# Performance work log

Measured on AMD Instinct MI355X. Metric: run time of the kernel, lower is better.

## Reference

```python
import jax, jax.numpy as jnp
import numpy as np

VOCAB, POS_V, NER_V, DEPREL_V = 50000, 50, 10, 40
EMB, POS_D, NER_D, MEM = 300, 30, 30, 200
NUM_LAYERS = 2


def setup_inputs() -> dict:
    key = jax.random.key(0)
    ks = jax.random.split(key, 12)
    B, L = 32, 100
    adj = jax.random.randint(ks[0], (B, L, L), 0, DEPREL_V)
    words = jax.random.randint(ks[1], (B, L), 0, VOCAB)
    pos = jax.random.randint(ks[2], (B, L), 0, POS_V)
    ner = jax.random.randint(ks[3], (B, L), 0, NER_V)
    s = 0.02
    emb = jax.random.normal(ks[4], (VOCAB, EMB), jnp.float32) * s
    pos_emb = jax.random.normal(ks[5], (POS_V, POS_D), jnp.float32) * s
    ner_emb = jax.random.normal(ks[6], (NER_V, NER_D), jnp.float32) * s
    deprel_emb = jax.random.normal(ks[7], (DEPREL_V, MEM), jnp.float32) * s
    deprel_emb = deprel_emb.at[0].set(0.0)  # padding_idx=0
    in_dim = EMB + POS_D + NER_D
    Wp = jax.random.normal(ks[8], (MEM, in_dim), jnp.float32) * s
    bp = jnp.zeros((MEM,), jnp.float32)
    W0 = jax.random.normal(ks[9], (MEM, MEM), jnp.float32) * s
    b0 = jnp.zeros((MEM,), jnp.float32)
    W1 = jax.random.normal(ks[10], (MEM, MEM), jnp.float32) * s
    b1 = jnp.zeros((MEM,), jnp.float32)
    return {"adj": adj, "words": words, "pos": pos, "ner": ner,
            "emb": emb, "pos_emb": pos_emb, "ner_emb": ner_emb,
            "deprel_emb": deprel_emb, "Wp": Wp, "bp": bp,
            "W0": W0, "b0": b0, "W1": W1, "b1": b1}


def reference(adj, words, pos, ner, emb, pos_emb, ner_emb, deprel_emb,
              Wp, bp, W0, b0, W1, b1):
    # embedding lookups + concat  -> [B, L, in_dim]
    embs = jnp.concatenate([emb[words], pos_emb[pos], ner_emb[ner]], axis=-1)
    # preprocessor linear (diagonal_deprel branch)  -> [B, L, D]
    x = embs @ Wp.T + bp
    # per-edge relation embedding gather  -> [B, L, L, D]
    deprel_adj = deprel_emb[adj]
    adj_m = (adj != 0).astype(jnp.float32)            # [B, L, L]
    denom = adj_m.sum(2)[..., None] + 1.0             # [B, L, 1]
    mask = ((adj_m.sum(2) + adj_m.sum(1)) == 0)[..., None]  # [B, L, 1]
    for W, b in ((W0, b0), (W1, b1)):
        # diagonal deprel aggregation: (deprel_adj * x[:,None]) summed over neighbors
        Ax = jnp.einsum('blmd,bmd->bld', deprel_adj, x)
        AxW = (Ax @ W.T + b) + (x @ W.T + b)
        x = jax.nn.relu(AxW / denom)
    return x, mask
```

## Files before the change

### kernel.cpp

```cpp
#include <hip/hip_runtime.h>
#include <hip/hip_bf16.h>

#define BB 32
#define LL 100
#define DD 200
#define KIN 360
#define NP (BB*LL)
#define RNUM 40
#define LT 13
#define NT 8

__device__ __forceinline__ void fma4(float4& a, const float4& w, float s) {
    a.x = fmaf(w.x, s, a.x);
    a.y = fmaf(w.y, s, a.y);
    a.z = fmaf(w.z, s, a.z);
    a.w = fmaf(w.w, s, a.w);
}
__device__ __forceinline__ unsigned bf16rn(float f) {
    unsigned u = __float_as_uint(f);
    return (u + 0x7fffu + ((u >> 16) & 1u)) >> 16;
}
__device__ __forceinline__ unsigned pk2(float a, float b) {
    return bf16rn(a) | (bf16rn(b) << 16);
}
__device__ __forceinline__ float lo16(unsigned u) { return __uint_as_float(u << 16); }
__device__ __forceinline__ float hi16(unsigned u) { return __uint_as_float(u & 0xffff0000u); }

__global__ __launch_bounds__(256) void prep_transpose_kernel(
        const int* __restrict__ adj,
        const float* __restrict__ Wp, const float* __restrict__ W0, const float* __restrict__ W1,
        float* __restrict__ WpT, float* __restrict__ W0T, float* __restrict__ W1T,
        float* __restrict__ invd, float* __restrict__ mask_out) {
    int bid = blockIdx.x, tid = threadIdx.x;
    if (bid < 25) {
        int t = bid * 256 + tid;
        int half = t & 1;
        int pl = t >> 1;
        int b = pl / LL, l = pl % LL;
        const int4* row = (const int4*)(adj + (size_t)pl * LL);
        int q0 = half ? 13 : 0, q1 = half ? 25 : 13;
        int rc = 0;
        for (int i = q0; i < q1; ++i) {
            int4 a = row[i];
            rc += (a.x != 0) + (a.y != 0) + (a.z != 0) + (a.w != 0);
        }
        const int* base = adj + (size_t)b * LL * LL + l;
        int cc = 0;
        for (int m = half * 50; m < half * 50 + 50; ++m) cc += (base[(size_t)m * LL] != 0);
        rc += __shfl_xor(rc, 1);
        cc += __shfl_xor(cc, 1);
        if (!half) {
            invd[pl] = 1.0f / (float)(rc + 1);
            mask_out[pl] = (rc + cc == 0) ? 1.0f : 0.0f;
        }
    } else {
        int i = (bid - 25) * 256 + tid;
        if (i < 18000) {
            int k = i / 50, o = (i % 50) * 4;
            float4 v;
            v.x = Wp[(size_t)(o + 0) * KIN + k];
            v.y = Wp[(size_t)(o + 1) * KIN + k];
            v.z = Wp[(size_t)(o + 2) * KIN + k];
            v.w = Wp[(size_t)(o + 3) * KIN + k];
            ((float4*)WpT)[i] = v;
        } else if (i < 28000) {
            int q = i - 18000;
            int k = q / 50, o = (q % 50) * 4;
            float4 v;
            v.x = W0[(size_t)(o + 0) * DD + k];
            v.y = W0[(size_t)(o + 1) * DD + k];
            v.z = W0[(size_t)(o + 2) * DD + k];
            v.w = W0[(size_t)(o + 3) * DD + k];
            ((float4*)W0T)[q] = v;
        } else if (i < 38000) {
            int q = i - 28000;
            int k = q / 50, o = (q % 50) * 4;
            float4 v;
            v.x = W1[(size_t)(o + 0) * DD + k];
            v.y = W1[(size_t)(o + 1) * DD + k];
            v.z = W1[(size_t)(o + 2) * DD + k];
            v.w = W1[(size_t)(o + 3) * DD + k];
            ((float4*)W1T)[q] = v;
        }
    }
}

__global__ __launch_bounds__(256) void embed_gemv_kernel(
        const int* __restrict__ words, const int* __restrict__ pos, const int* __restrict__ ner,
        const float* __restrict__ emb, const float* __restrict__ pose, const float* __restrict__ nere,
        const float* __restrict__ wpt, const float* __restrict__ bp,
        float* __restrict__ xA) {
    __shared__ float es[8 * KIN];
    __shared__ float4 red[4 * 8 * 50];
    int tid = threadIdx.x;
    int pbase = blockIdx.x * 8;

    float2* es2 = (float2*)es;
    for (int idx = tid; idx < 8 * 180; idx += 256) {
        int p = idx / 180, j2 = idx % 180;
        int gp = pbase + p;
        float2 v;
        if (j2 < 150)      v = ((const float2*)emb)[(size_t)words[gp] * 150 + j2];
        else if (j2 < 165) v = ((const float2*)pose)[pos[gp] * 15 + (j2 - 150)];
        else               v = ((const float2*)nere)[ner[gp] * 15 + (j2 - 165)];
        es2[idx] = v;
    }
    __syncthreads();

    int lane = tid & 63, w = tid >> 6;
    bool act = lane < 50;
    int oq = act ? lane : 49;
    int kq0 = w * 24;
    int npair = (w < 3) ? 12 : 9;
    int kqlast = kq0 + 2 * npair - 1;
    const float4* wt4 = (const float4*)wpt;
    const float4* es4 = (const float4*)es;

    float4 a[8];
    #pragma unroll
    for (int p = 0; p < 8; ++p) a[p] = make_float4(0.f, 0.f, 0.f, 0.f);

    float4 wc[8], wn[8];
    #pragma unroll
    for (int q = 0; q < 2; ++q)
        #pragma unroll
        for (int j = 0; j < 4; ++j)
            wc[q * 4 + j] = wt4[(size_t)(4 * (kq0 + q) + j) * 50 + oq];

    for (int pr = 0; pr < npair; ++pr) {
        int nb = kq0 + 2 * pr + 2;
        int nbA = nb <= kqlast ? nb : kq0;
        int nbB = nb + 1 <= kqlast ? nb + 1 : kq0;
        #pragma unroll
        for (int j = 0; j < 4; ++j) wn[j]     = wt4[(size_t)(4 * nbA + j) * 50 + oq];
        #pragma unroll
        for (int j = 0; j < 4; ++j) wn[4 + j] = wt4[(size_t)(4 * nbB + j) * 50 + oq];
        #pragma unroll
        for (int q = 0; q < 2; ++q) {
            int kq = kq0 + 2 * pr + q;
            #pragma unroll
            for (int p = 0; p < 8; ++p) {
                float4 s = es4[p * 90 + kq];
                fma4(a[p], wc[q * 4 + 0], s.x); fma4(a[p], wc[q * 4 + 1], s.y);
                fma4(a[p], wc[q * 4 + 2], s.z); fma4(a[p], wc[q * 4 + 3], s.w);
            }
        }
        #pragma unroll
        for (int j = 0; j < 8; ++j) wc[j] = wn[j];
    }

    if (act) {
        #pragma unroll
        for (int p = 0; p < 8; ++p) red[w * 400 + p * 50 + oq] = a[p];
    }
    __syncthreads();
    for (int t = tid; t < 400; t += 256) {
        int oq2 = t % 50;
        float4 v0 = red[t], v1 = red[400 + t], v2 = red[800 + t], v3 = red[1200 + t];
        float4 bb = ((const float4*)bp)[oq2];
        float4 v;
        v.x = v0.x + v1.x + v2.x + v3.x + bb.x;
        v.y = v0.y + v1.y + v2.y + v3.y + bb.y;
        v.z = v0.z + v1.z + v2.z + v3.z + bb.z;
        v.w = v0.w + v1.w + v2.w + v3.w + bb.w;
        ((float4*)xA)[(size_t)(pbase + t / 50) * 50 + oq2] = v;
    }
}

__global__ __launch_bounds__(512) void layer_kernel(
        const float* __restrict__ x, const int* __restrict__ adj,
        const float* __restrict__ deprel, const float* __restrict__ wt,
        const float* __restrict__ bias, const float* __restrict__ invd,
        float* __restrict__ out) {
    __shared__ uint2 deps_b[RNUM * 50];
    __shared__ unsigned adjp[LT * 25];
    __shared__ float4 Sh[2 * 650];
    __shared__ float4 Sfin[650];
    int b = blockIdx.y, tile = blockIdx.x;
    int l0 = tile * LT;
    int lcnt = min(LT, LL - l0);
    int tid = threadIdx.x;
    const float4* x4 = (const float4*)x;

    for (int i = tid; i < RNUM * 50; i += 512) {
        float4 v = ((const float4*)deprel)[i];
        deps_b[i] = make_uint2(pk2(v.x, v.y), pk2(v.z, v.w));
    }
    for (int i = tid; i < lcnt * 25; i += 512) {
        int li = i / 25, mg = i % 25;
        int4 a = ((const int4*)(adj + (size_t)(b * LL + l0 + li) * LL))[mg];
        adjp[i] = (unsigned)a.x | ((unsigned)a.y << 8) | ((unsigned)a.z << 16) | ((unsigned)a.w << 24);
    }
    __syncthreads();

    int lane = tid & 63, w = tid >> 6;
    int lg = w & 3, mh = w >> 2;
    bool act = lane < 50;
    int dq = lane;

    float4 acc[4];
    #pragma unroll
    for (int i = 0; i < 4; ++i) acc[i] = make_float4(0.f, 0.f, 0.f, 0.f);
    if (act) {
        int mg0 = mh ? 13 : 0, mg1 = mh ? 25 : 13;
        float4 xc[4], xn[4];
        #pragma unroll
        for (int mm = 0; mm < 4; ++mm)
            xc[mm] = x4[(size_t)(b * LL + 4 * mg0 + mm) * 50 + dq];
        for (int mg = mg0; mg < mg1; ++mg) {
            int mgn = (mg + 1 < mg1) ? mg + 1 : mg;
            #pragma unroll
            for (int mm = 0; mm < 4; ++mm)
                xn[mm] = x4[(size_t)(b * LL + 4 * mgn + mm) * 50 + dq];
            unsigned ap[4];
            #pragma unroll
            for (int i = 0; i < 4; ++i) {
                int li = lg + 4 * i;
                ap[i] = (li < lcnt) ? adjp[li * 25 + mg] : 0u;
            }
            #pragma unroll
            for (int mm = 0; mm < 4; ++mm) {
                #pragma unroll
                for (int i = 0; i < 4; ++i) {
                    unsigned r = (ap[i] >> (8 * mm)) & 0xffu;
                    uint2 dv = deps_b[r * 50 + dq];
                    acc[i].x = fmaf(lo16(dv.x), xc[mm].x, acc[i].x);
                    acc[i].y = fmaf(hi16(dv.x), xc[mm].y, acc[i].y);
                    acc[i].z = fmaf(lo16(dv.y), xc[mm].z, acc[i].z);
                    acc[i].w = fmaf(hi16(dv.y), xc[mm].w, acc[i].w);
                }
            }
            #pragma unroll
            for (int mm = 0; mm < 4; ++mm) xc[mm] = xn[mm];
        }
        #pragma unroll
        for (int i = 0; i < 4; ++i) {
            int li = lg + 4 * i;
            if (li < lcnt) Sh[mh * 650 + li * 50 + dq] = acc[i];
        }
    }
    __syncthreads();

    for (int t2 = tid; t2 < 650; t2 += 512) {
        int li = t2 / 50;
        if (li < lcnt) {
            float4 s0 = Sh[t2], s1 = Sh[650 + t2];
            float4 xr = x4[(size_t)(b * LL + l0 + li) * 50 + (t2 % 50)];
            float4 s;
            s.x = s0.x + s1.x + xr.x; s.y = s0.y + s1.y + xr.y;
            s.z = s0.z + s1.z + xr.z; s.w = s0.w + s1.w + xr.w;
            Sfin[t2] = s;
        }
    }
    __syncthreads();

    const float4* wt4 = (const float4*)wt;
    int oq = act ? lane : 49;
    int kq0 = mh * 25;
    float4 ba[4];
    #pragma unroll
    for (int i = 0; i < 4; ++i) ba[i] = make_float4(0.f, 0.f, 0.f, 0.f);

    float4 wc[8], wn[8];
    #pragma unroll
    for (int q = 0; q < 2; ++q)
        #pragma unroll
        for (int j = 0; j < 4; ++j)
            wc[q * 4 + j] = wt4[(size_t)(4 * (kq0 + q) + j) * 50 + oq];

    int lic[4];
    #pragma unroll
    for (int i = 0; i < 4; ++i) {
        int li = lg + 4 * i;
        lic[i] = li < lcnt ? li : lcnt - 1;
    }

    for (int pr = 0; pr < 12; ++pr) {
        int nb = kq0 + 2 * pr + 2;
        int nbB = (nb + 1 <= kq0 + 24) ? nb + 1 : kq0;
        #pragma unroll
        for (int j = 0; j < 4; ++j) wn[j]     = wt4[(size_t)(4 * nb + j) * 50 + oq];
        #pragma unroll
        for (int j = 0; j < 4; ++j) wn[4 + j] = wt4[(size_t)(4 * nbB + j) * 50 + oq];
        #pragma unroll
        for (int q = 0; q < 2; ++q) {
            int kq = kq0 + 2 * pr + q;
            #pragma unroll
            for (int i = 0; i < 4; ++i) {
                float4 s = Sfin[lic[i] * 50 + kq];
                fma4(ba[i], wc[q * 4 + 0], s.x); fma4(ba[i], wc[q * 4 + 1], s.y);
                fma4(ba[i], wc[q * 4 + 2], s.z); fma4(ba[i], wc[q * 4 + 3], s.w);
            }
        }
        #pragma unroll
        for (int j = 0; j < 8; ++j) wc[j] = wn[j];
    }
    {
        int kq = kq0 + 24;
        #pragma unroll
        for (int i = 0; i < 4; ++i) {
            float4 s = Sfin[lic[i] * 50 + kq];
            fma4(ba[i], wc[0], s.x); fma4(ba[i], wc[1], s.y);
            fma4(ba[i], wc[2], s.z); fma4(ba[i], wc[3], s.w);
        }
    }

    if (act) {
        #pragma unroll
        for (int i = 0; i < 4; ++i) {
            int li = lg + 4 * i;
            if (li < lcnt) Sh[mh * 650 + li * 50 + oq] = ba[i];
        }
    }
    __syncthreads();

    for (int t2 = tid; t2 < 650; t2 += 512) {
        int li = t2 / 50, oq2 = t2 % 50;
        if (li < lcnt) {
            float4 v0 = Sh[t2], v1 = Sh[650 + t2];
            float4 bb = ((const float4*)bias)[oq2];
            int p = b * LL + l0 + li;
            float sc = invd[p];
            float4 v;
            v.x = fmaxf((v0.x + v1.x + 2.f * bb.x) * sc, 0.f);
            v.y = fmaxf((v0.y + v1.y + 2.f * bb.y) * sc, 0.f);
            v.z = fmaxf((v0.z + v1.z + 2.f * bb.z) * sc, 0.f);
            v.w = fmaxf((v0.w + v1.w + 2.f * bb.w) * sc, 0.f);
            ((float4*)out)[(size_t)p * 50 + oq2] = v;
        }
    }
}

extern "C" void kernel_launch(void* const* d_in, const int* in_sizes, int n_in,
                              void* d_out, int out_size, void* d_ws, size_t ws_size,
                              hipStream_t stream) {
    const int*   adj   = (const int*)d_in[0];
    const int*   words = (const int*)d_in[1];
    const int*   pos   = (const int*)d_in[2];
    const int*   ner   = (const int*)d_in[3];
    const float* emb   = (const float*)d_in[4];
    const float* pose  = (const float*)d_in[5];
    const float* nere  = (const float*)d_in[6];
    const float* dep   = (const float*)d_in[7];
    const float* Wp    = (const float*)d_in[8];
    const float* bp    = (const float*)d_in[9];
    const float* W0    = (const float*)d_in[10];
    const float* b0    = (const float*)d_in[11];
    const float* W1    = (const float*)d_in[12];
    const float* b1    = (const float*)d_in[13];
    float* out = (float*)d_out;
    float* ws  = (float*)d_ws;

    float* xA   = ws;
    float* xB   = ws + 640000;
    float* WpT  = ws + 1280000;
    float* W0T  = ws + 1352000;
    float* W1T  = ws + 1392000;
    float* invd = ws + 1432000;

    prep_transpose_kernel<<<25 + 149, 256, 0, stream>>>(adj, Wp, W0, W1, WpT, W0T, W1T,
                                                        invd, out + (size_t)NP * DD);
    embed_gemv_kernel<<<NP / 8, 256, 0, stream>>>(words, pos, ner, emb, pose, nere,
                                                  WpT, bp, xA);
    layer_kernel<<<dim3(NT, BB), 512, 0, stream>>>(xA, adj, dep, W0T, b0, invd, xB);
    layer_kernel<<<dim3(NT, BB), 512, 0, stream>>>(xB, adj, dep, W1T, b1, invd, out);
}
```

Measured before the change: 74.09 us.

## Double block sizes and split reductions across more wavefronts in embed and layer kernels

Embed GEMV blocks grow from 256 to 512 threads, splitting the K dimension over 8 wavefronts instead of 4, with an 8-way shared-memory reduction. Layer blocks grow from 512 to 1024 threads, splitting the neighbor aggregation and the weight GEMV over 4 slices instead of 2. Shared memory is overlaid into a single buffer so Sfin reuses the deprel table space. The aim is more in-flight wavefronts per block for the small 256-block grid, at the cost of larger reductions, more register pressure under the new launch bounds, and one more sync's worth of partial-sum traffic.

```diff
diff --git a/kernel.cpp b/kernel.cpp
--- a/kernel.cpp
+++ b/kernel.cpp
@@ -85,18 +85,18 @@
     }
 }
 
-__global__ __launch_bounds__(256) void embed_gemv_kernel(
+__global__ __launch_bounds__(512, 4) void embed_gemv_kernel(
         const int* __restrict__ words, const int* __restrict__ pos, const int* __restrict__ ner,
         const float* __restrict__ emb, const float* __restrict__ pose, const float* __restrict__ nere,
         const float* __restrict__ wpt, const float* __restrict__ bp,
         float* __restrict__ xA) {
     __shared__ float es[8 * KIN];
-    __shared__ float4 red[4 * 8 * 50];
+    __shared__ float4 red[8 * 8 * 50];
     int tid = threadIdx.x;
     int pbase = blockIdx.x * 8;
 
     float2* es2 = (float2*)es;
-    for (int idx = tid; idx < 8 * 180; idx += 256) {
+    for (int idx = tid; idx < 8 * 180; idx += 512) {
         int p = idx / 180, j2 = idx % 180;
         int gp = pbase + p;
         float2 v;
@@ -110,8 +110,8 @@
     int lane = tid & 63, w = tid >> 6;
     bool act = lane < 50;
     int oq = act ? lane : 49;
-    int kq0 = w * 24;
-    int npair = (w < 3) ? 12 : 9;
+    int kq0 = (w < 5) ? 12 * w : 60 + 10 * (w - 5);
+    int npair = (w < 5) ? 6 : 5;
     int kqlast = kq0 + 2 * npair - 1;
     const float4* wt4 = (const float4*)wpt;
     const float4* es4 = (const float4*)es;
@@ -154,39 +154,40 @@
         for (int p = 0; p < 8; ++p) red[w * 400 + p * 50 + oq] = a[p];
     }
     __syncthreads();
-    for (int t = tid; t < 400; t += 256) {
+    for (int t = tid; t < 400; t += 512) {
         int oq2 = t % 50;
-        float4 v0 = red[t], v1 = red[400 + t], v2 = red[800 + t], v3 = red[1200 + t];
-        float4 bb = ((const float4*)bp)[oq2];
-        float4 v;
-        v.x = v0.x + v1.x + v2.x + v3.x + bb.x;
-        v.y = v0.y + v1.y + v2.y + v3.y + bb.y;
-        v.z = v0.z + v1.z + v2.z + v3.z + bb.z;
-        v.w = v0.w + v1.w + v2.w + v3.w + bb.w;
+        float4 v = ((const float4*)bp)[oq2];
+        #pragma unroll
+        for (int s = 0; s < 8; ++s) {
+            float4 r = red[s * 400 + t];
+            v.x += r.x; v.y += r.y; v.z += r.z; v.w += r.w;
+        }
         ((float4*)xA)[(size_t)(pbase + t / 50) * 50 + oq2] = v;
     }
 }
 
-__global__ __launch_bounds__(512) void layer_kernel(
+__global__ __launch_bounds__(1024, 4) void layer_kernel(
         const float* __restrict__ x, const int* __restrict__ adj,
         const float* __restrict__ deprel, const float* __restrict__ wt,
         const float* __restrict__ bias, const float* __restrict__ invd,
         float* __restrict__ out) {
-    __shared__ uint2 deps_b[RNUM * 50];
-    __shared__ unsigned adjp[LT * 25];
-    __shared__ float4 Sh[2 * 650];
-    __shared__ float4 Sfin[650];
+    __shared__ alignas(16) char smem[58912];
+    uint2* deps_b = (uint2*)smem;
+    unsigned* adjp = (unsigned*)(smem + 16000);
+    float4* Sh = (float4*)(smem + 17312);
+    float4* Sfin = (float4*)smem;
+
     int b = blockIdx.y, tile = blockIdx.x;
     int l0 = tile * LT;
     int lcnt = min(LT, LL - l0);
     int tid = threadIdx.x;
     const float4* x4 = (const float4*)x;
 
-    for (int i = tid; i < RNUM * 50; i += 512) {
+    for (int i = tid; i < RNUM * 50; i += 1024) {
         float4 v = ((const float4*)deprel)[i];
         deps_b[i] = make_uint2(pk2(v.x, v.y), pk2(v.z, v.w));
     }
-    for (int i = tid; i < lcnt * 25; i += 512) {
+    for (int i = tid; i < lcnt * 25; i += 1024) {
         int li = i / 25, mg = i % 25;
         int4 a = ((const int4*)(adj + (size_t)(b * LL + l0 + li) * LL))[mg];
         adjp[i] = (unsigned)a.x | ((unsigned)a.y << 8) | ((unsigned)a.z << 16) | ((unsigned)a.w << 24);
@@ -194,7 +195,7 @@
     __syncthreads();
 
     int lane = tid & 63, w = tid >> 6;
-    int lg = w & 3, mh = w >> 2;
+    int lg = w & 3, sq = w >> 2;
     bool act = lane < 50;
     int dq = lane;
 
@@ -202,7 +203,8 @@
     #pragma unroll
     for (int i = 0; i < 4; ++i) acc[i] = make_float4(0.f, 0.f, 0.f, 0.f);
     if (act) {
-        int mg0 = mh ? 13 : 0, mg1 = mh ? 25 : 13;
+        int mg0 = (sq == 0) ? 0 : 1 + 6 * sq;
+        int mg1 = mg0 + ((sq == 0) ? 7 : 6);
         float4 xc[4], xn[4];
         #pragma unroll
         for (int mm = 0; mm < 4; ++mm)
@@ -236,19 +238,21 @@
         #pragma unroll
         for (int i = 0; i < 4; ++i) {
             int li = lg + 4 * i;
-            if (li < lcnt) Sh[mh * 650 + li * 50 + dq] = acc[i];
-        }
-    }
-    __syncthreads();
-
-    for (int t2 = tid; t2 < 650; t2 += 512) {
+            if (li < lcnt) Sh[sq * 650 + li * 50 + dq] = acc[i];
+        }
+    }
+    __syncthreads();
+
+    for (int t2 = tid; t2 < 650; t2 += 1024) {
         int li = t2 / 50;
         if (li < lcnt) {
-            float4 s0 = Sh[t2], s1 = Sh[650 + t2];
+            float4 s0 = Sh[t2], s1 = Sh[650 + t2], s2 = Sh[1300 + t2], s3 = Sh[1950 + t2];
             float4 xr = x4[(size_t)(b * LL + l0 + li) * 50 + (t2 % 50)];
             float4 s;
-            s.x = s0.x + s1.x + xr.x; s.y = s0.y + s1.y + xr.y;
-            s.z = s0.z + s1.z + xr.z; s.w = s0.w + s1.w + xr.w;
+            s.x = s0.x + s1.x + s2.x + s3.x + xr.x;
+            s.y = s0.y + s1.y + s2.y + s3.y + xr.y;
+            s.z = s0.z + s1.z + s2.z + s3.z + xr.z;
+            s.w = s0.w + s1.w + s2.w + s3.w + xr.w;
             Sfin[t2] = s;
         }
     }
@@ -256,7 +260,10 @@
 
     const float4* wt4 = (const float4*)wt;
     int oq = act ? lane : 49;
-    int kq0 = mh * 25;
+    int kq0 = (sq < 2) ? 13 * sq : 26 + 12 * (sq - 2);
+    int kcnt = (sq < 2) ? 13 : 12;
+    int npair = kcnt >> 1;
+    int kqlast = kq0 + kcnt - 1;
     float4 ba[4];
     #pragma unroll
     for (int i = 0; i < 4; ++i) ba[i] = make_float4(0.f, 0.f, 0.f, 0.f);
@@ -275,11 +282,12 @@
         lic[i] = li < lcnt ? li : lcnt - 1;
     }
 
-    for (int pr = 0; pr < 12; ++pr) {
+    for (int pr = 0; pr < npair; ++pr) {
         int nb = kq0 + 2 * pr + 2;
-        int nbB = (nb + 1 <= kq0 + 24) ? nb + 1 : kq0;
-        #pragma unroll
-        for (int j = 0; j < 4; ++j) wn[j]     = wt4[(size_t)(4 * nb + j) * 50 + oq];
+        int nbA = nb <= kqlast ? nb : kq0;
+        int nbB = nb + 1 <= kqlast ? nb + 1 : kq0;
+        #pragma unroll
+        for (int j = 0; j < 4; ++j) wn[j]     = wt4[(size_t)(4 * nbA + j) * 50 + oq];
         #pragma unroll
         for (int j = 0; j < 4; ++j) wn[4 + j] = wt4[(size_t)(4 * nbB + j) * 50 + oq];
         #pragma unroll
@@ -295,11 +303,10 @@
         #pragma unroll
         for (int j = 0; j < 8; ++j) wc[j] = wn[j];
     }
-    {
-        int kq = kq0 + 24;
+    if (kcnt & 1) {
         #pragma unroll
         for (int i = 0; i < 4; ++i) {
-            float4 s = Sfin[lic[i] * 50 + kq];
+            float4 s = Sfin[lic[i] * 50 + kqlast];
             fma4(ba[i], wc[0], s.x); fma4(ba[i], wc[1], s.y);
             fma4(ba[i], wc[2], s.z); fma4(ba[i], wc[3], s.w);
         }
@@ -309,23 +316,23 @@
         #pragma unroll
         for (int i = 0; i < 4; ++i) {
             int li = lg + 4 * i;
-            if (li < lcnt) Sh[mh * 650 + li * 50 + oq] = ba[i];
-        }
-    }
-    __syncthreads();
-
-    for (int t2 = tid; t2 < 650; t2 += 512) {
+            if (li < lcnt) Sh[sq * 650 + li * 50 + oq] = ba[i];
+        }
+    }
+    __syncthreads();
+
+    for (int t2 = tid; t2 < 650; t2 += 1024) {
         int li = t2 / 50, oq2 = t2 % 50;
         if (li < lcnt) {
-            float4 v0 = Sh[t2], v1 = Sh[650 + t2];
+            float4 v0 = Sh[t2], v1 = Sh[650 + t2], v2 = Sh[1300 + t2], v3 = Sh[1950 + t2];
             float4 bb = ((const float4*)bias)[oq2];
             int p = b * LL + l0 + li;
             float sc = invd[p];
             float4 v;
-            v.x = fmaxf((v0.x + v1.x + 2.f * bb.x) * sc, 0.f);
-            v.y = fmaxf((v0.y + v1.y + 2.f * bb.y) * sc, 0.f);
-            v.z = fmaxf((v0.z + v1.z + 2.f * bb.z) * sc, 0.f);
-            v.w = fmaxf((v0.w + v1.w + 2.f * bb.w) * sc, 0.f);
+            v.x = fmaxf((v0.x + v1.x + v2.x + v3.x + 2.f * bb.x) * sc, 0.f);
+            v.y = fmaxf((v0.y + v1.y + v2.y + v3.y + 2.f * bb.y) * sc, 0.f);
+            v.z = fmaxf((v0.z + v1.z + v2.z + v3.z + 2.f * bb.z) * sc, 0.f);
+            v.w = fmaxf((v0.w + v1.w + v2.w + v3.w + 2.f * bb.w) * sc, 0.f);
             ((float4*)out)[(size_t)p * 50 + oq2] = v;
         }
     }
@@ -360,8 +367,8 @@
 
     prep_transpose_kernel<<<25 + 149, 256, 0, stream>>>(adj, Wp, W0, W1, WpT, W0T, W1T,
                                                         invd, out + (size_t)NP * DD);
-    embed_gemv_kernel<<<NP / 8, 256, 0, stream>>>(words, pos, ner, emb, pose, nere,
+    embed_gemv_kernel<<<NP / 8, 512, 0, stream>>>(words, pos, ner, emb, pose, nere,
                                                   WpT, bp, xA);
-    layer_kernel<<<dim3(NT, BB), 512, 0, stream>>>(xA, adj, dep, W0T, b0, invd, xB);
-    layer_kernel<<<dim3(NT, BB), 512, 0, stream>>>(xB, adj, dep, W1T, b1, invd, out);
-}
+    layer_kernel<<<dim3(NT, BB), 1024, 0, stream>>>(xA, adj, dep, W0T, b0, invd, xB);
+    layer_kernel<<<dim3(NT, BB), 1024, 0, stream>>>(xB, adj, dep, W1T, b1, invd, out);
+}
```

New measurement: 69.80 us. -5.8%, faster.
